# Performance work log

Measured on AMD Instinct MI355X. Metric: run time of the kernel, lower is better.

The kernel has to match this reference:

```python
import jax, jax.numpy as jnp
import numpy as np

B, N, FIN, FOUT, K = 8, 1024, 32, 4, 2
FREQS = [2.0, 3.0, 4.0, 5.0]  # q_idx = 1/FREQS[idx]


def setup_inputs() -> dict:
    key = jax.random.key(0)
    k1, k2, k3, k4, k5 = jax.random.split(key, 5)
    X_real = jax.random.normal(k1, (B, N, FIN), jnp.float32)
    X_imag = jax.random.normal(k2, (B, N, FIN), jnp.float32)
    adj = jax.random.uniform(k3, (B, N, N), jnp.float32)  # weighted directed adjacency
    stdv = 1.0 / np.sqrt(FIN)
    weight = jax.random.uniform(k4, (FOUT, K + 1, FIN), jnp.float32, -stdv, stdv)
    bias = jax.random.uniform(k5, (FOUT,), jnp.float32, -stdv, stdv)
    return {"X_real": X_real, "X_imag": X_imag, "adj": adj, "weight": weight, "bias": bias}


def _mag_laplacian(adj, q):
    """Normalized magnetic Laplacian, real/imag parts. adj: [B,N,N]."""
    adj_t = jnp.swapaxes(adj, -1, -2)
    As = 0.5 * (adj + adj_t)                    # symmetrized adjacency
    D = As.sum(-1)                              # degrees [B,N]
    dinv = jnp.where(D > 0, 1.0 / jnp.sqrt(jnp.where(D > 0, D, 1.0)), 0.0)
    theta = (2.0 * np.pi * q) * (adj - adj_t)   # phase matrix
    S = dinv[:, :, None] * As * dinv[:, None, :]  # D^-1/2 As D^-1/2
    I = jnp.eye(N, dtype=adj.dtype)
    L_real = I - S * jnp.cos(theta)
    L_imag = -S * jnp.sin(theta)
    return L_real, L_imag


def _cmatvec(Lr, Li, zr, zi):
    """Complex batched matmul (Lr+iLi) @ (zr+izi); L:[B,N,N], z:[B,N,F]."""
    return Lr @ zr - Li @ zi, Li @ zr + Lr @ zi


def reference(X_real, X_imag, adj, weight, bias):
    outs_r, outs_i = [], []
    for idx in range(FOUT):  # small fixed loop over output channels / frequencies
        q = 1.0 / FREQS[idx]
        Lr, Li = _mag_laplacian(adj, q)
        # Chebyshev polynomials applied directly to the signal:
        # T0 = I -> z0 = X ; T1 = I - L -> z1 = X - L X ; T_k = 2 L T_{k-1} + T_{k-2}
        z = [(X_real, X_imag)]
        hr, hi = _cmatvec(Lr, Li, X_real, X_imag)
        z.append((X_real - hr, X_imag - hi))
        for i in range(2, K + 1):
            mr, mi = _cmatvec(Lr, Li, z[i - 1][0], z[i - 1][1])
            z.append((2.0 * mr + z[i - 2][0], 2.0 * mi + z[i - 2][1]))
        Zr = jnp.stack([t[0] for t in z], 0)  # [K+1, B, N, FIN]
        Zi = jnp.stack([t[1] for t in z], 0)
        or_ = jnp.einsum('kbnf,kf->bn', Zr, weight[idx]) + bias[idx]
        oi_ = jnp.einsum('kbnf,kf->bn', Zi, weight[idx])
        outs_r.append(or_)
        outs_i.append(oi_)
    return jnp.stack(outs_r, -1), jnp.stack(outs_i, -1)  # each [B, N, FOUT]
```

## Files before the change

### kernel.cpp

```cpp
#include <hip/hip_runtime.h>
#include <cstddef>

#define NB 8
#define NN 1024
#define NF 32
#define NIDX 4
#define JC 4
#define JCH 256
#define NJT 4

#define OFF_ROW   0u
#define OFF_COLP  8192u
#define OFF_DINV  532480u
#define OFF_S     540672u
#define OFF_P     606208u
#define OFF_R     671744u
#define OFF_WP    737280u

#if __has_builtin(__builtin_amdgcn_sinf)
#define FSIN(x) __builtin_amdgcn_sinf(x)
#define FCOS(x) __builtin_amdgcn_cosf(x)
#else
#define FSIN(x) __sinf((x) * 6.283185307179586f)
#define FCOS(x) __cosf((x) * 6.283185307179586f)
#endif

__global__ __launch_bounds__(512) void k_sums(const float* __restrict__ adj,
                                              float* __restrict__ rowsum,
                                              float* __restrict__ colpart,
                                              float* __restrict__ out) {
  int b = blockIdx.x, strip = blockIdx.y;
  int t = threadIdx.x, lane = t & 63, w = t >> 6;
  { int zid = blockIdx.x*64 + blockIdx.y;
    if (t < 128) out[zid*128 + t] = 0.f; }
  float colreg[16];
  #pragma unroll
  for (int i = 0; i < 16; ++i) colreg[i] = 0.f;
  int r0 = strip*16 + w*2;
  #pragma unroll
  for (int rr = 0; rr < 2; ++rr) {
    const float4* row4 = reinterpret_cast<const float4*>(adj + ((size_t)b*NN + r0 + rr)*NN);
    float rs = 0.f;
    #pragma unroll
    for (int cq = 0; cq < 4; ++cq) {
      float4 v = row4[cq*64 + lane];
      colreg[cq*4+0] += v.x; colreg[cq*4+1] += v.y;
      colreg[cq*4+2] += v.z; colreg[cq*4+3] += v.w;
      rs += (v.x + v.y) + (v.z + v.w);
    }
    #pragma unroll
    for (int o = 32; o > 0; o >>= 1) rs += __shfl_xor(rs, o);
    if (lane == 0) rowsum[b*NN + r0 + rr] = rs;
  }
  __shared__ float cacc[8][NN];
  #pragma unroll
  for (int cq = 0; cq < 4; ++cq)
    #pragma unroll
    for (int x = 0; x < 4; ++x) cacc[w][cq*256 + lane*4 + x] = colreg[cq*4+x];
  __syncthreads();
  for (int c = t; c < NN; c += 512) {
    float s = 0.f;
    #pragma unroll
    for (int ww = 0; ww < 8; ++ww) s += cacc[ww][c];
    colpart[(size_t)strip*(NB*NN) + b*NN + c] = s;
  }
}

__global__ __launch_bounds__(256) void k_prep(const float* __restrict__ Xr, const float* __restrict__ Xi,
                       const float* __restrict__ weight,
                       const float* __restrict__ rowsum, const float* __restrict__ colpart,
                       float* __restrict__ dinv,
                       float* __restrict__ svec, float* __restrict__ pvec, float* __restrict__ rvec) {
  __shared__ float wsm[NIDX*3*NF];
  int t = threadIdx.x;
  for (int e = t; e < NIDX*3*NF; e += 256) wsm[e] = weight[e];
  __syncthreads();
  int gid = blockIdx.x*256 + t;
  float cs = 0.f;
  for (int k = 0; k < 64; ++k) cs += colpart[(size_t)k*(NB*NN) + gid];
  float D = 0.5f*(rowsum[gid] + cs);
  float di = (D > 0.f) ? (1.0f / sqrtf(D)) : 0.f;
  dinv[gid] = di;
  const float* xr = Xr + (size_t)gid*NF;
  const float* xi = Xi + (size_t)gid*NF;
  float acc[NIDX][3][2];
  #pragma unroll
  for (int x = 0; x < NIDX; ++x)
    #pragma unroll
    for (int v = 0; v < 3; ++v) { acc[x][v][0] = 0.f; acc[x][v][1] = 0.f; }
  for (int f = 0; f < NF; ++f) {
    float xrf = xr[f], xif = xi[f];
    #pragma unroll
    for (int x = 0; x < NIDX; ++x) {
      float w0 = wsm[x*96 + f], w1 = wsm[x*96 + 32 + f], w2 = wsm[x*96 + 64 + f];
      float av = w0 + w2, bv = w1 + 2.f*w2, cv = -2.f*w2;
      acc[x][0][0] += av*xrf; acc[x][0][1] += av*xif;
      acc[x][1][0] += bv*xrf; acc[x][1][1] += bv*xif;
      acc[x][2][0] += cv*xrf; acc[x][2][1] += cv*xif;
    }
  }
  #pragma unroll
  for (int x = 0; x < NIDX; ++x) {
    size_t o = (size_t)gid*8 + x*2;
    svec[o] = acc[x][0][0];      svec[o+1] = acc[x][0][1];
    pvec[o] = acc[x][1][0];      pvec[o+1] = acc[x][1][1];
    rvec[o] = di*acc[x][2][0];   rvec[o+1] = di*acc[x][2][1];
  }
}

template<int MODE>
__global__ __launch_bounds__(512, 4) void k_pass(const float* __restrict__ adj,
                                                 const float* __restrict__ dinv,
                                                 const float* __restrict__ vin,
                                                 float* __restrict__ wpart,
                                                 const float* __restrict__ svec,
                                                 const float* __restrict__ bias,
                                                 float* __restrict__ out) {
  __shared__ float Tjs[64][65];
  __shared__ float vlds[JCH][8];
  __shared__ float red[8][8*72];
  int b = blockIdx.y, i0 = blockIdx.x*64, zc = blockIdx.z;
  int j0base = zc*JCH;
  int t = threadIdx.x, lane = t & 63;
  int w = t >> 6;
  int wu = __builtin_amdgcn_readfirstlane(w);
  const float QV[NIDX] = {0.5f, 1.f/3.f, 0.25f, 0.2f};

  if constexpr (MODE == 1) {
    for (int e = t; e < JCH*8; e += 512) {
      int jj = e >> 3, s = e & 7;
      size_t o = ((size_t)b*NN + j0base + jj)*8 + s;
      float v = vin[o];
      #pragma unroll
      for (int c = 0; c < JC; ++c) v += wpart[(size_t)c*65536 + o];
      vlds[jj][s] = v * dinv[b*NN + j0base + jj];
    }
  }

  float accr[8][NIDX], acci[8][NIDX];
  #pragma unroll
  for (int s = 0; s < 8; ++s)
    #pragma unroll
    for (int x = 0; x < NIDX; ++x) { accr[s][x] = 0.f; acci[s][x] = 0.f; }

  for (int jt = 0; jt < NJT; ++jt) {
    int j0 = j0base + jt*64;
    __syncthreads();
    #pragma unroll
    for (int m = 0; m < 2; ++m) {
      int e4 = t + 512*m;
      int jj = e4 >> 4, i4 = (e4 & 15) << 2;
      float4 vv = *reinterpret_cast<const float4*>(adj + ((size_t)b*NN + j0 + jj)*NN + i0 + i4);
      float* dst = &Tjs[jj][i4];
      dst[0] = vv.x; dst[1] = vv.y; dst[2] = vv.z; dst[3] = vv.w;
    }
    float vr[NIDX], vi[NIDX];
    if constexpr (MODE == 0) {
      const float4* vb = reinterpret_cast<const float4*>(vin + ((size_t)b*NN + j0 + lane)*8);
      float4 a = vb[0], c = vb[1];
      vr[0]=a.x; vi[0]=a.y; vr[1]=a.z; vi[1]=a.w;
      vr[2]=c.x; vi[2]=c.y; vr[3]=c.z; vi[3]=c.w;
    } else {
      const float4* vb = reinterpret_cast<const float4*>(&vlds[jt*64 + lane][0]);
      float4 a = vb[0], c = vb[1];
      vr[0]=a.x; vi[0]=a.y; vr[1]=a.z; vi[1]=a.w;
      vr[2]=c.x; vi[2]=c.y; vr[3]=c.z; vi[3]=c.w;
    }
    __syncthreads();
    const float* arbase = adj + ((size_t)b*NN + i0 + wu*8)*NN + j0 + lane;
    #pragma unroll
    for (int s = 0; s < 8; ++s) {
      float ar = arbase[(size_t)s*NN];
      float ac = Tjs[lane][wu*8 + s];
      float dd = ar - ac, sm = ar + ac;
      #pragma unroll
      for (int x = 0; x < NIDX; ++x) {
        float u = QV[x]*dd;
        float sn = FSIN(u), cw = FCOS(u);
        float tr = cw*vr[x] - sn*vi[x];
        float ti = cw*vi[x] + sn*vr[x];
        accr[s][x] += sm*tr;
        acci[s][x] += sm*ti;
      }
    }
  }

  bool b1 = (lane & 1), b2 = (lane & 2), b4 = (lane & 4);
  #pragma unroll
  for (int s = 0; s < 8; ++s) {
    float v0 = accr[s][0], v1 = acci[s][0], v2 = accr[s][1], v3 = acci[s][1];
    float v4 = accr[s][2], v5 = acci[s][2], v6 = accr[s][3], v7 = acci[s][3];
    float k0 = b1 ? v1 : v0, s0 = b1 ? v0 : v1;
    float k1 = b1 ? v3 : v2, s1 = b1 ? v2 : v3;
    float k2 = b1 ? v5 : v4, s2 = b1 ? v4 : v5;
    float k3 = b1 ? v7 : v6, s3 = b1 ? v6 : v7;
    v0 = k0 + __shfl_xor(s0, 1);
    v1 = k1 + __shfl_xor(s1, 1);
    v2 = k2 + __shfl_xor(s2, 1);
    v3 = k3 + __shfl_xor(s3, 1);
    k0 = b2 ? v1 : v0; s0 = b2 ? v0 : v1;
    k1 = b2 ? v3 : v2; s1 = b2 ? v2 : v3;
    v0 = k0 + __shfl_xor(s0, 2);
    v1 = k1 + __shfl_xor(s1, 2);
    k0 = b4 ? v1 : v0; s0 = b4 ? v0 : v1;
    v0 = k0 + __shfl_xor(s0, 4);
    red[w][s*72 + (lane & 7)*9 + (lane >> 3)] = v0;
  }
  __syncthreads();
  {
    int iloc = w*8 + (lane >> 3), slot = lane & 7;
    float sum = 0.f;
    #pragma unroll
    for (int g = 0; g < 8; ++g) sum += red[w][(lane >> 3)*72 + slot*9 + g];
    int i = i0 + iloc;
    float val = sum * 0.5f * dinv[b*NN + i];
    if constexpr (MODE == 0) {
      wpart[(size_t)zc*65536 + ((size_t)b*NN + i)*8 + slot] = val;
    } else {
      if (zc == 0) {
        val += svec[((size_t)b*NN + i)*8 + slot];
        if ((slot & 1) == 0) val += bias[slot >> 1];
      }
      atomicAdd(&out[(slot & 1)*32768 + b*4096 + i*4 + (slot >> 1)], val);
    }
  }
}

extern "C" void kernel_launch(void* const* d_in, const int* in_sizes, int n_in,
                              void* d_out, int out_size, void* d_ws, size_t ws_size,
                              hipStream_t stream) {
  (void)in_sizes; (void)n_in; (void)out_size; (void)ws_size;
  const float* Xr     = (const float*)d_in[0];
  const float* Xi     = (const float*)d_in[1];
  const float* adj    = (const float*)d_in[2];
  const float* weight = (const float*)d_in[3];
  const float* bias   = (const float*)d_in[4];
  float* ws = (float*)d_ws;
  float* rowsum  = ws + OFF_ROW;
  float* colpart = ws + OFF_COLP;
  float* dinv    = ws + OFF_DINV;
  float* svec    = ws + OFF_S;
  float* pvec    = ws + OFF_P;
  float* rvec    = ws + OFF_R;
  float* wpart   = ws + OFF_WP;
  float* out = (float*)d_out;

  k_sums<<<dim3(NB, 64), 512, 0, stream>>>(adj, rowsum, colpart, out);
  k_prep<<<dim3(NB*NN/256), 256, 0, stream>>>(Xr, Xi, weight, rowsum, colpart, dinv, svec, pvec, rvec);
  k_pass<0><<<dim3(NN/64, NB, JC), 512, 0, stream>>>(adj, dinv, rvec, wpart, svec, bias, out);
  k_pass<1><<<dim3(NN/64, NB, JC), 512, 0, stream>>>(adj, dinv, pvec, wpart, svec, bias, out);
}
```

Before: 56.18 us.

## Exploit Hermitian symmetry by processing only upper-triangular tile pairs

The pass kernels now launch one block per upper-triangular (i,j) 64x64 tile pair and use each adj tile for both the i-row and the conjugate j-row contributions. This roughly halves adjacency reads and sin/cos evaluations. Partial results are accumulated with atomics, and a new small mid kernel combines pvec with the partial sums and initialises the output with svec plus bias. The costs are more atomics, an extra launch, a serial loop to decode the pair index, extra registers and LDS, and a diagonal branch.

```diff
diff --git a/kernel.cpp b/kernel.cpp
--- a/kernel.cpp
+++ b/kernel.cpp
@@ -5,9 +5,8 @@
 #define NN 1024
 #define NF 32
 #define NIDX 4
-#define JC 4
-#define JCH 256
-#define NJT 4
+#define NTILE 16
+#define NPAIR 136
 
 #define OFF_ROW   0u
 #define OFF_COLP  8192u
@@ -16,6 +15,7 @@
 #define OFF_P     606208u
 #define OFF_R     671744u
 #define OFF_WP    737280u
+#define OFF_WT    802816u
 
 #if __has_builtin(__builtin_amdgcn_sinf)
 #define FSIN(x) __builtin_amdgcn_sinf(x)
@@ -28,11 +28,11 @@
 __global__ __launch_bounds__(512) void k_sums(const float* __restrict__ adj,
                                               float* __restrict__ rowsum,
                                               float* __restrict__ colpart,
-                                              float* __restrict__ out) {
+                                              float* __restrict__ wpart) {
   int b = blockIdx.x, strip = blockIdx.y;
   int t = threadIdx.x, lane = t & 63, w = t >> 6;
   { int zid = blockIdx.x*64 + blockIdx.y;
-    if (t < 128) out[zid*128 + t] = 0.f; }
+    if (t < 128) wpart[zid*128 + t] = 0.f; }
   float colreg[16];
   #pragma unroll
   for (int i = 0; i < 16; ++i) colreg[i] = 0.f;
@@ -108,79 +108,79 @@
   }
 }
 
+__global__ void k_mid(const float* __restrict__ dinv, const float* __restrict__ pvec,
+                      const float* __restrict__ wpart, const float* __restrict__ svec,
+                      const float* __restrict__ bias, float* __restrict__ wtot,
+                      float* __restrict__ out) {
+  int o = blockIdx.x*256 + threadIdx.x;
+  int g = o >> 3, slot = o & 7, x = slot >> 1, p = slot & 1;
+  wtot[o] = dinv[g] * (pvec[o] + wpart[o]);
+  out[p*32768 + g*4 + x] = svec[o] + (p ? 0.f : bias[x]);
+}
+
 template<int MODE>
 __global__ __launch_bounds__(512, 4) void k_pass(const float* __restrict__ adj,
                                                  const float* __restrict__ dinv,
                                                  const float* __restrict__ vin,
-                                                 float* __restrict__ wpart,
-                                                 const float* __restrict__ svec,
-                                                 const float* __restrict__ bias,
-                                                 float* __restrict__ out) {
+                                                 float* __restrict__ outacc) {
   __shared__ float Tjs[64][65];
-  __shared__ float vlds[JCH][8];
-  __shared__ float red[8][8*72];
-  int b = blockIdx.y, i0 = blockIdx.x*64, zc = blockIdx.z;
-  int j0base = zc*JCH;
-  int t = threadIdx.x, lane = t & 63;
-  int w = t >> 6;
+  __shared__ float redI[8][8*72];
+  __shared__ float redJ[8][64*9];
+  int b = blockIdx.y;
+  int pid = blockIdx.x;
+  int ti = 0, rem = pid;
+  while (rem >= NTILE - ti) { rem -= NTILE - ti; ++ti; }
+  int tj = ti + rem;
+  bool diag = (ti == tj);
+  int i0 = ti*64, j0 = tj*64;
+  int t = threadIdx.x, lane = t & 63, w = t >> 6;
   int wu = __builtin_amdgcn_readfirstlane(w);
   const float QV[NIDX] = {0.5f, 1.f/3.f, 0.25f, 0.2f};
 
-  if constexpr (MODE == 1) {
-    for (int e = t; e < JCH*8; e += 512) {
-      int jj = e >> 3, s = e & 7;
-      size_t o = ((size_t)b*NN + j0base + jj)*8 + s;
-      float v = vin[o];
-      #pragma unroll
-      for (int c = 0; c < JC; ++c) v += wpart[(size_t)c*65536 + o];
-      vlds[jj][s] = v * dinv[b*NN + j0base + jj];
-    }
-  }
+  #pragma unroll
+  for (int m = 0; m < 2; ++m) {
+    int e4 = t + 512*m;
+    int jj = e4 >> 4, i4 = (e4 & 15) << 2;
+    float4 vv = *reinterpret_cast<const float4*>(adj + ((size_t)b*NN + j0 + jj)*NN + i0 + i4);
+    float* dst = &Tjs[jj][i4];
+    dst[0] = vv.x; dst[1] = vv.y; dst[2] = vv.z; dst[3] = vv.w;
+  }
+  const float4* vb = reinterpret_cast<const float4*>(vin + ((size_t)b*NN + j0 + lane)*8);
+  float4 a4 = vb[0], c4 = vb[1];
+  float vrj[NIDX] = {a4.x, a4.z, c4.x, c4.z};
+  float vij[NIDX] = {a4.y, a4.w, c4.y, c4.w};
+  __syncthreads();
 
   float accr[8][NIDX], acci[8][NIDX];
   #pragma unroll
   for (int s = 0; s < 8; ++s)
     #pragma unroll
     for (int x = 0; x < NIDX; ++x) { accr[s][x] = 0.f; acci[s][x] = 0.f; }
-
-  for (int jt = 0; jt < NJT; ++jt) {
-    int j0 = j0base + jt*64;
-    __syncthreads();
-    #pragma unroll
-    for (int m = 0; m < 2; ++m) {
-      int e4 = t + 512*m;
-      int jj = e4 >> 4, i4 = (e4 & 15) << 2;
-      float4 vv = *reinterpret_cast<const float4*>(adj + ((size_t)b*NN + j0 + jj)*NN + i0 + i4);
-      float* dst = &Tjs[jj][i4];
-      dst[0] = vv.x; dst[1] = vv.y; dst[2] = vv.z; dst[3] = vv.w;
-    }
-    float vr[NIDX], vi[NIDX];
-    if constexpr (MODE == 0) {
-      const float4* vb = reinterpret_cast<const float4*>(vin + ((size_t)b*NN + j0 + lane)*8);
-      float4 a = vb[0], c = vb[1];
-      vr[0]=a.x; vi[0]=a.y; vr[1]=a.z; vi[1]=a.w;
-      vr[2]=c.x; vi[2]=c.y; vr[3]=c.z; vi[3]=c.w;
-    } else {
-      const float4* vb = reinterpret_cast<const float4*>(&vlds[jt*64 + lane][0]);
-      float4 a = vb[0], c = vb[1];
-      vr[0]=a.x; vi[0]=a.y; vr[1]=a.z; vi[1]=a.w;
-      vr[2]=c.x; vi[2]=c.y; vr[3]=c.z; vi[3]=c.w;
-    }
-    __syncthreads();
-    const float* arbase = adj + ((size_t)b*NN + i0 + wu*8)*NN + j0 + lane;
-    #pragma unroll
-    for (int s = 0; s < 8; ++s) {
-      float ar = arbase[(size_t)s*NN];
-      float ac = Tjs[lane][wu*8 + s];
-      float dd = ar - ac, sm = ar + ac;
-      #pragma unroll
-      for (int x = 0; x < NIDX; ++x) {
-        float u = QV[x]*dd;
-        float sn = FSIN(u), cw = FCOS(u);
-        float tr = cw*vr[x] - sn*vi[x];
-        float ti = cw*vi[x] + sn*vr[x];
-        accr[s][x] += sm*tr;
-        acci[s][x] += sm*ti;
+  float jar[NIDX] = {0.f,0.f,0.f,0.f}, jai[NIDX] = {0.f,0.f,0.f,0.f};
+
+  const float* arbase = adj + ((size_t)b*NN + i0 + wu*8)*NN + j0 + lane;
+  const float* vibase = vin + ((size_t)b*NN + i0 + wu*8)*8;
+  #pragma unroll
+  for (int s = 0; s < 8; ++s) {
+    float ar = arbase[(size_t)s*NN];
+    float ac = Tjs[lane][wu*8 + s];
+    float dd = ar - ac, sm = ar + ac;
+    float vri[NIDX], vii[NIDX];
+    #pragma unroll
+    for (int x = 0; x < NIDX; ++x) { vri[x] = vibase[s*8 + x*2]; vii[x] = vibase[s*8 + x*2 + 1]; }
+    #pragma unroll
+    for (int x = 0; x < NIDX; ++x) {
+      float u = QV[x]*dd;
+      float sn = FSIN(u), cw = FCOS(u);
+      float tr = cw*vrj[x] - sn*vij[x];
+      float tii = cw*vij[x] + sn*vrj[x];
+      accr[s][x] += sm*tr;
+      acci[s][x] += sm*tii;
+      if (!diag) {
+        float trc = cw*vri[x] + sn*vii[x];
+        float tic = cw*vii[x] - sn*vri[x];
+        jar[x] += sm*trc;
+        jai[x] += sm*tic;
       }
     }
   }
@@ -204,25 +204,35 @@
     v1 = k1 + __shfl_xor(s1, 2);
     k0 = b4 ? v1 : v0; s0 = b4 ? v0 : v1;
     v0 = k0 + __shfl_xor(s0, 4);
-    red[w][s*72 + (lane & 7)*9 + (lane >> 3)] = v0;
+    redI[w][s*72 + (lane & 7)*9 + (lane >> 3)] = v0;
+  }
+  if (!diag) {
+    #pragma unroll
+    for (int x = 0; x < NIDX; ++x) {
+      redJ[w][lane*9 + x*2]     = jar[x];
+      redJ[w][lane*9 + x*2 + 1] = jai[x];
+    }
   }
   __syncthreads();
   {
     int iloc = w*8 + (lane >> 3), slot = lane & 7;
     float sum = 0.f;
     #pragma unroll
-    for (int g = 0; g < 8; ++g) sum += red[w][(lane >> 3)*72 + slot*9 + g];
-    int i = i0 + iloc;
-    float val = sum * 0.5f * dinv[b*NN + i];
-    if constexpr (MODE == 0) {
-      wpart[(size_t)zc*65536 + ((size_t)b*NN + i)*8 + slot] = val;
-    } else {
-      if (zc == 0) {
-        val += svec[((size_t)b*NN + i)*8 + slot];
-        if ((slot & 1) == 0) val += bias[slot >> 1];
-      }
-      atomicAdd(&out[(slot & 1)*32768 + b*4096 + i*4 + (slot >> 1)], val);
-    }
+    for (int g = 0; g < 8; ++g) sum += redI[w][(lane >> 3)*72 + slot*9 + g];
+    int gi = b*NN + i0 + iloc;
+    float val = sum * 0.5f * dinv[gi];
+    if constexpr (MODE == 0) atomicAdd(&outacc[(size_t)gi*8 + slot], val);
+    else                     atomicAdd(&outacc[(slot & 1)*32768 + gi*4 + (slot >> 1)], val);
+  }
+  if (!diag) {
+    int jloc = t >> 3, slot = t & 7;
+    float sum = 0.f;
+    #pragma unroll
+    for (int ww = 0; ww < 8; ++ww) sum += redJ[ww][jloc*9 + slot];
+    int gj = b*NN + j0 + jloc;
+    float val = sum * 0.5f * dinv[gj];
+    if constexpr (MODE == 0) atomicAdd(&outacc[(size_t)gj*8 + slot], val);
+    else                     atomicAdd(&outacc[(slot & 1)*32768 + gj*4 + (slot >> 1)], val);
   }
 }
 
@@ -243,10 +253,12 @@
   float* pvec    = ws + OFF_P;
   float* rvec    = ws + OFF_R;
   float* wpart   = ws + OFF_WP;
+  float* wtot    = ws + OFF_WT;
   float* out = (float*)d_out;
 
-  k_sums<<<dim3(NB, 64), 512, 0, stream>>>(adj, rowsum, colpart, out);
+  k_sums<<<dim3(NB, 64), 512, 0, stream>>>(adj, rowsum, colpart, wpart);
   k_prep<<<dim3(NB*NN/256), 256, 0, stream>>>(Xr, Xi, weight, rowsum, colpart, dinv, svec, pvec, rvec);
-  k_pass<0><<<dim3(NN/64, NB, JC), 512, 0, stream>>>(adj, dinv, rvec, wpart, svec, bias, out);
-  k_pass<1><<<dim3(NN/64, NB, JC), 512, 0, stream>>>(adj, dinv, pvec, wpart, svec, bias, out);
-}
+  k_pass<0><<<dim3(NPAIR, NB), 512, 0, stream>>>(adj, dinv, rvec, wpart);
+  k_mid<<<dim3(256), 256, 0, stream>>>(dinv, pvec, wpart, svec, bias, wtot, out);
+  k_pass<1><<<dim3(NPAIR, NB), 512, 0, stream>>>(adj, dinv, wtot, out);
+}
```

New measurement: 65.33 us. 16.3% more time.

## Shrink pass tiles, atomically reduce j-chunks, and derive sin/cos via double-angle

Applied to the files above, without the earlier changes.

The pass kernels now use 256-thread blocks covering 16 output rows instead of 64, which quadruples the grid. Partial sums across j-chunks are now combined with atomicAdd into a single zeroed wpart buffer, replacing per-chunk slices that the second pass had to reduce in a preamble. The base term and bias are written directly to the output by the prep kernel, so the svec buffer goes away. For q=1/2, sin and cos are computed from the q=1/4 values with double-angle identities, saving one transcendental pair per element at a small accuracy cost. The extra atomics and smaller tiles mean less reuse of the transposed adjacency tile per load.

```diff
diff --git a/kernel.cpp b/kernel.cpp
--- a/kernel.cpp
+++ b/kernel.cpp
@@ -5,6 +5,8 @@
 #define NN 1024
 #define NF 32
 #define NIDX 4
+#define TIR 16
+#define WIR 4
 #define JC 4
 #define JCH 256
 #define NJT 4
@@ -12,10 +14,9 @@
 #define OFF_ROW   0u
 #define OFF_COLP  8192u
 #define OFF_DINV  532480u
-#define OFF_S     540672u
-#define OFF_P     606208u
-#define OFF_R     671744u
-#define OFF_WP    737280u
+#define OFF_P     540672u
+#define OFF_R     606208u
+#define OFF_WP    671744u
 
 #if __has_builtin(__builtin_amdgcn_sinf)
 #define FSIN(x) __builtin_amdgcn_sinf(x)
@@ -28,11 +29,11 @@
 __global__ __launch_bounds__(512) void k_sums(const float* __restrict__ adj,
                                               float* __restrict__ rowsum,
                                               float* __restrict__ colpart,
-                                              float* __restrict__ out) {
+                                              float* __restrict__ wpart) {
   int b = blockIdx.x, strip = blockIdx.y;
   int t = threadIdx.x, lane = t & 63, w = t >> 6;
   { int zid = blockIdx.x*64 + blockIdx.y;
-    if (t < 128) out[zid*128 + t] = 0.f; }
+    if (t < 128) wpart[zid*128 + t] = 0.f; }
   float colreg[16];
   #pragma unroll
   for (int i = 0; i < 16; ++i) colreg[i] = 0.f;
@@ -69,8 +70,10 @@
 __global__ __launch_bounds__(256) void k_prep(const float* __restrict__ Xr, const float* __restrict__ Xi,
                        const float* __restrict__ weight,
                        const float* __restrict__ rowsum, const float* __restrict__ colpart,
+                       const float* __restrict__ bias,
                        float* __restrict__ dinv,
-                       float* __restrict__ svec, float* __restrict__ pvec, float* __restrict__ rvec) {
+                       float* __restrict__ pvec, float* __restrict__ rvec,
+                       float* __restrict__ out) {
   __shared__ float wsm[NIDX*3*NF];
   int t = threadIdx.x;
   for (int e = t; e < NIDX*3*NF; e += 256) wsm[e] = weight[e];
@@ -102,92 +105,86 @@
   #pragma unroll
   for (int x = 0; x < NIDX; ++x) {
     size_t o = (size_t)gid*8 + x*2;
-    svec[o] = acc[x][0][0];      svec[o+1] = acc[x][0][1];
     pvec[o] = acc[x][1][0];      pvec[o+1] = acc[x][1][1];
     rvec[o] = di*acc[x][2][0];   rvec[o+1] = di*acc[x][2][1];
+    out[gid*4 + x]         = acc[x][0][0] + bias[x];
+    out[32768 + gid*4 + x] = acc[x][0][1];
   }
 }
 
 template<int MODE>
-__global__ __launch_bounds__(512, 4) void k_pass(const float* __restrict__ adj,
+__global__ __launch_bounds__(256, 4) void k_pass(const float* __restrict__ adj,
                                                  const float* __restrict__ dinv,
                                                  const float* __restrict__ vin,
-                                                 float* __restrict__ wpart,
-                                                 const float* __restrict__ svec,
-                                                 const float* __restrict__ bias,
-                                                 float* __restrict__ out) {
-  __shared__ float Tjs[64][65];
-  __shared__ float vlds[JCH][8];
-  __shared__ float red[8][8*72];
-  int b = blockIdx.y, i0 = blockIdx.x*64, zc = blockIdx.z;
-  int j0base = zc*JCH;
-  int t = threadIdx.x, lane = t & 63;
-  int w = t >> 6;
+                                                 const float* __restrict__ pvec,
+                                                 const float* __restrict__ wpart,
+                                                 float* __restrict__ outacc) {
+  __shared__ float Tjs[64][17];
+  __shared__ float red[4][WIR*72];
+  int b = blockIdx.y, i0 = blockIdx.x*TIR, zc = blockIdx.z;
+  int t = threadIdx.x, lane = t & 63, w = t >> 6;
   int wu = __builtin_amdgcn_readfirstlane(w);
-  const float QV[NIDX] = {0.5f, 1.f/3.f, 0.25f, 0.2f};
-
-  if constexpr (MODE == 1) {
-    for (int e = t; e < JCH*8; e += 512) {
-      int jj = e >> 3, s = e & 7;
-      size_t o = ((size_t)b*NN + j0base + jj)*8 + s;
-      float v = vin[o];
-      #pragma unroll
-      for (int c = 0; c < JC; ++c) v += wpart[(size_t)c*65536 + o];
-      vlds[jj][s] = v * dinv[b*NN + j0base + jj];
-    }
-  }
-
-  float accr[8][NIDX], acci[8][NIDX];
-  #pragma unroll
-  for (int s = 0; s < 8; ++s)
+  float accr[WIR][NIDX], acci[WIR][NIDX];
+  #pragma unroll
+  for (int s = 0; s < WIR; ++s)
     #pragma unroll
     for (int x = 0; x < NIDX; ++x) { accr[s][x] = 0.f; acci[s][x] = 0.f; }
 
   for (int jt = 0; jt < NJT; ++jt) {
-    int j0 = j0base + jt*64;
+    int j0 = zc*JCH + jt*64;
     __syncthreads();
-    #pragma unroll
-    for (int m = 0; m < 2; ++m) {
-      int e4 = t + 512*m;
-      int jj = e4 >> 4, i4 = (e4 & 15) << 2;
+    {
+      int jj = t >> 2, i4 = (t & 3) << 2;
       float4 vv = *reinterpret_cast<const float4*>(adj + ((size_t)b*NN + j0 + jj)*NN + i0 + i4);
       float* dst = &Tjs[jj][i4];
       dst[0] = vv.x; dst[1] = vv.y; dst[2] = vv.z; dst[3] = vv.w;
     }
+    int gj = b*NN + j0 + lane;
     float vr[NIDX], vi[NIDX];
     if constexpr (MODE == 0) {
-      const float4* vb = reinterpret_cast<const float4*>(vin + ((size_t)b*NN + j0 + lane)*8);
+      const float4* vb = reinterpret_cast<const float4*>(vin + (size_t)gj*8);
       float4 a = vb[0], c = vb[1];
       vr[0]=a.x; vi[0]=a.y; vr[1]=a.z; vi[1]=a.w;
       vr[2]=c.x; vi[2]=c.y; vr[3]=c.z; vi[3]=c.w;
     } else {
-      const float4* vb = reinterpret_cast<const float4*>(&vlds[jt*64 + lane][0]);
-      float4 a = vb[0], c = vb[1];
-      vr[0]=a.x; vi[0]=a.y; vr[1]=a.z; vi[1]=a.w;
-      vr[2]=c.x; vi[2]=c.y; vr[3]=c.z; vi[3]=c.w;
+      const float4* pb = reinterpret_cast<const float4*>(pvec + (size_t)gj*8);
+      const float4* wb = reinterpret_cast<const float4*>(wpart + (size_t)gj*8);
+      float4 p0 = pb[0], p1 = pb[1], w0 = wb[0], w1 = wb[1];
+      float dj = dinv[gj];
+      vr[0]=dj*(p0.x+w0.x); vi[0]=dj*(p0.y+w0.y);
+      vr[1]=dj*(p0.z+w0.z); vi[1]=dj*(p0.w+w0.w);
+      vr[2]=dj*(p1.x+w1.x); vi[2]=dj*(p1.y+w1.y);
+      vr[3]=dj*(p1.z+w1.z); vi[3]=dj*(p1.w+w1.w);
     }
     __syncthreads();
-    const float* arbase = adj + ((size_t)b*NN + i0 + wu*8)*NN + j0 + lane;
-    #pragma unroll
-    for (int s = 0; s < 8; ++s) {
-      float ar = arbase[(size_t)s*NN];
-      float ac = Tjs[lane][wu*8 + s];
+    const float* arb = adj + ((size_t)b*NN + i0 + wu*WIR)*NN + j0 + lane;
+    #pragma unroll
+    for (int s = 0; s < WIR; ++s) {
+      float ar = arb[(size_t)s*NN];
+      float ac = Tjs[lane][wu*WIR + s];
       float dd = ar - ac, sm = ar + ac;
+      float snv[NIDX], csv[NIDX];
+      float u4 = 0.25f*dd;
+      snv[2] = FSIN(u4); csv[2] = FCOS(u4);
+      float s4sq = snv[2]*snv[2];
+      csv[0] = 1.f - 2.f*s4sq;
+      snv[0] = 2.f*snv[2]*csv[2];
+      float u1 = (1.f/3.f)*dd;
+      snv[1] = FSIN(u1); csv[1] = FCOS(u1);
+      float u3 = 0.2f*dd;
+      snv[3] = FSIN(u3); csv[3] = FCOS(u3);
       #pragma unroll
       for (int x = 0; x < NIDX; ++x) {
-        float u = QV[x]*dd;
-        float sn = FSIN(u), cw = FCOS(u);
-        float tr = cw*vr[x] - sn*vi[x];
-        float ti = cw*vi[x] + sn*vr[x];
-        accr[s][x] += sm*tr;
-        acci[s][x] += sm*ti;
+        float A = sm*csv[x], B = sm*snv[x];
+        accr[s][x] += A*vr[x] - B*vi[x];
+        acci[s][x] += A*vi[x] + B*vr[x];
       }
     }
   }
 
   bool b1 = (lane & 1), b2 = (lane & 2), b4 = (lane & 4);
   #pragma unroll
-  for (int s = 0; s < 8; ++s) {
+  for (int s = 0; s < WIR; ++s) {
     float v0 = accr[s][0], v1 = acci[s][0], v2 = accr[s][1], v3 = acci[s][1];
     float v4 = accr[s][2], v5 = acci[s][2], v6 = accr[s][3], v7 = acci[s][3];
     float k0 = b1 ? v1 : v0, s0 = b1 ? v0 : v1;
@@ -207,22 +204,15 @@
     red[w][s*72 + (lane & 7)*9 + (lane >> 3)] = v0;
   }
   __syncthreads();
-  {
-    int iloc = w*8 + (lane >> 3), slot = lane & 7;
+  if (t < TIR*8) {
+    int row = t >> 3, slot = t & 7;
     float sum = 0.f;
     #pragma unroll
-    for (int g = 0; g < 8; ++g) sum += red[w][(lane >> 3)*72 + slot*9 + g];
-    int i = i0 + iloc;
-    float val = sum * 0.5f * dinv[b*NN + i];
-    if constexpr (MODE == 0) {
-      wpart[(size_t)zc*65536 + ((size_t)b*NN + i)*8 + slot] = val;
-    } else {
-      if (zc == 0) {
-        val += svec[((size_t)b*NN + i)*8 + slot];
-        if ((slot & 1) == 0) val += bias[slot >> 1];
-      }
-      atomicAdd(&out[(slot & 1)*32768 + b*4096 + i*4 + (slot >> 1)], val);
-    }
+    for (int g = 0; g < 8; ++g) sum += red[row >> 2][(row & 3)*72 + slot*9 + g];
+    int gi = b*NN + i0 + row;
+    float val = sum * 0.5f * dinv[gi];
+    if constexpr (MODE == 0) atomicAdd(&outacc[(size_t)gi*8 + slot], val);
+    else atomicAdd(&outacc[(slot & 1)*32768 + gi*4 + (slot >> 1)], val);
   }
 }
 
@@ -239,14 +229,14 @@
   float* rowsum  = ws + OFF_ROW;
   float* colpart = ws + OFF_COLP;
   float* dinv    = ws + OFF_DINV;
-  float* svec    = ws + OFF_S;
   float* pvec    = ws + OFF_P;
   float* rvec    = ws + OFF_R;
   float* wpart   = ws + OFF_WP;
   float* out = (float*)d_out;
 
-  k_sums<<<dim3(NB, 64), 512, 0, stream>>>(adj, rowsum, colpart, out);
-  k_prep<<<dim3(NB*NN/256), 256, 0, stream>>>(Xr, Xi, weight, rowsum, colpart, dinv, svec, pvec, rvec);
-  k_pass<0><<<dim3(NN/64, NB, JC), 512, 0, stream>>>(adj, dinv, rvec, wpart, svec, bias, out);
-  k_pass<1><<<dim3(NN/64, NB, JC), 512, 0, stream>>>(adj, dinv, pvec, wpart, svec, bias, out);
-}
+  k_sums<<<dim3(NB, 64), 512, 0, stream>>>(adj, rowsum, colpart, wpart);
+  k_prep<<<dim3(NB*NN/256), 256, 0, stream>>>(Xr, Xi, weight, rowsum, colpart, bias,
+                                              dinv, pvec, rvec, out);
+  k_pass<0><<<dim3(NN/TIR, NB, JC), 256, 0, stream>>>(adj, dinv, rvec, pvec, wpart, wpart);
+  k_pass<1><<<dim3(NN/TIR, NB, JC), 256, 0, stream>>>(adj, dinv, rvec, pvec, wpart, out);
+}
```

After: 70.43 us. +25.4%, slower.
